# Kernel tuning notes

Hardware: AMD Instinct MI355X
Metric: run time of the kernel (lower is better)

Reference implementation:

```python
import jax, jax.numpy as jnp
import numpy as np

ALPHA = 0.2
NEG_INF = -9e15


def setup_inputs() -> dict:
    key = jax.random.key(0)
    k1, k2, k3, k4 = jax.random.split(key, 4)
    B, N, C_IN, C_OUT, R, H = 8, 1024, 256, 256, 4, 4
    node_feats = jax.random.normal(k1, (B, N, C_IN), dtype=jnp.float32)
    adj_matrix = jax.random.randint(k2, (B, N, N, R), 0, 2, dtype=jnp.int32)
    # xavier_uniform with gain=1.414 for Linear(c_in, c_out) weights
    lim_w = 1.414 * np.sqrt(6.0 / (C_IN + C_OUT))
    W = jax.random.uniform(k3, (R, C_IN, C_OUT), minval=-lim_w, maxval=lim_w, dtype=jnp.float32)
    c_per = C_OUT // H
    lim_a = 1.414 * np.sqrt(6.0 / (H + 2 * c_per))
    a = jax.random.uniform(k4, (R, H, 2 * c_per), minval=-lim_a, maxval=lim_a, dtype=jnp.float32)
    return {"node_feats": node_feats, "adj_matrix": adj_matrix, "W": W, "a": a}


def reference(node_feats, adj_matrix, W, a):
    B, N, _ = node_feats.shape
    R, H = a.shape[0], a.shape[1]
    C = a.shape[2] // 2  # per-head feature dim
    out = jnp.zeros((B, N, H, C), dtype=node_feats.dtype)
    for r in range(R):
        # per-relation projection: [B,N,H,C]
        f = jnp.einsum('bnc,cd->bnd', node_feats, W[r]).reshape(B, N, H, C)
        a_l, a_r = a[r, :, :C], a[r, :, C:]
        # attention logit decomposes: a . [f_i || f_j] = a_l . f_i + a_r . f_j
        li = jnp.einsum('bnhc,hc->bnh', f, a_l)  # source-node term
        lj = jnp.einsum('bnhc,hc->bnh', f, a_r)  # target-node term
        logits = jax.nn.leaky_relu(li[:, :, None, :] + lj[:, None, :, :], ALPHA)  # [B,N,N,H]
        mask = adj_matrix[..., r] != 0  # [B,N,N]
        logits = jnp.where(mask[..., None], logits, NEG_INF)
        probs = jax.nn.softmax(logits, axis=2)
        out = out + jnp.einsum('bijh,bjhc->bihc', probs, f)
    # concat_heads=True
    return out.reshape(B, N, H * C)
```

## Files before the change

### kernel.cpp

```cpp
#include <hip/hip_runtime.h>
#include <math.h>

#define Bsz 8
#define Nn 1024
#define CIN 256
#define COUT 256
#define NR 4
#define NH 4

typedef unsigned short u16;
typedef __attribute__((ext_vector_type(8))) short bf16x8;
typedef __attribute__((ext_vector_type(4))) float f32x4;
typedef __attribute__((ext_vector_type(2))) float f32x2;

#define OFF_LIP (16u << 20)
#define OFF_LJP ((16u << 20) + (512u << 10))
#define OFF_ADJM (17u << 20)
#define OFF_XBF (21u << 20)
#define OFF_WFRAG (25u << 20)
#define OFF_WAL ((25u << 20) + (512u << 10))
#define OFF_WAR ((25u << 20) + (528u << 10))

#define LOG2E 1.4426950408889634f

__device__ __forceinline__ short f2bf(float x) {
  union { float f; unsigned u; } v; v.f = x;
  unsigned r = (v.u + 0x7FFFu + ((v.u >> 16) & 1u)) >> 16;
  return (short)r;
}

__device__ __forceinline__ float fast_exp2(float x) {
#if __has_builtin(__builtin_amdgcn_exp2f)
  return __builtin_amdgcn_exp2f(x);
#else
  return exp2f(x);
#endif
}

__device__ __forceinline__ int sbfe1(unsigned v, int bit) {
#if __has_builtin(__builtin_amdgcn_sbfe)
  return __builtin_amdgcn_sbfe((int)v, bit, 1);
#else
  return ((int)(v << (31 - bit))) >> 31;
#endif
}

__device__ __forceinline__ unsigned perm_hi16(unsigned hi, unsigned lo) {
#if __has_builtin(__builtin_amdgcn_perm)
  return __builtin_amdgcn_perm(hi, lo, 0x07060302u);
#else
  return (lo >> 16) | (hi & 0xFFFF0000u);
#endif
}

__global__ __launch_bounds__(256, 4)
void gatt_packprep(const int4* __restrict__ adj4, const float* __restrict__ W,
                   const float* __restrict__ a, unsigned long long* __restrict__ adjm,
                   u16* __restrict__ Wfrag, float* __restrict__ wa_l,
                   float* __restrict__ wa_r) {
  const int t = threadIdx.x;
  if (blockIdx.x < 32768) {
    const int wid = blockIdx.x * 4 + (t >> 6);
    const int lane = t & 63;
    const int jw = wid & 15;
    const int i = (wid >> 4) & 1023;
    const int b = wid >> 14;
    const int j = jw * 64 + lane;
    const int4 av = adj4[(size_t)(b * Nn + i) * Nn + j];
    const unsigned long long b0 = __ballot(av.x != 0);
    const unsigned long long b1 = __ballot(av.y != 0);
    const unsigned long long b2 = __ballot(av.z != 0);
    const unsigned long long b3 = __ballot(av.w != 0);
    if (lane < 4) {
      unsigned long long v = (lane == 0) ? b0 : (lane == 1) ? b1 : (lane == 2) ? b2 : b3;
      adjm[((size_t)((b * Nn + i) * NR + lane)) * 16 + jw] = v;
    }
  } else if (blockIdx.x < 32768 + 32) {
    const int bid2 = blockIdx.x - 32768;
    const int r = bid2 >> 3, kc = bid2 & 7;
    const int cg = t >> 4, mm = t & 15;
    float wv[32];
#pragma unroll 8
    for (int kk = 0; kk < 32; ++kk)
      wv[kk] = W[(size_t)r * 65536 + (size_t)(kc * 32 + kk) * COUT + t];
    u16* base = Wfrag + (size_t)r * 65536 + (size_t)(cg * 8 + kc) * 512 + mm * 8;
#pragma unroll
    for (int quad = 0; quad < 4; ++quad) {
      u16 pk[8];
#pragma unroll
      for (int e = 0; e < 8; ++e) pk[e] = (u16)f2bf(wv[quad * 8 + e]);
      *(int4*)(base + quad * 128) = *(int4*)pk;
    }
  } else {
    const int cb = blockIdx.x - 32768 - 32;
    const int r = cb >> 2, h = cb & 3;
    float sl = 0.f, sr = 0.f;
    const float* Wp = W + (size_t)r * 65536 + (size_t)t * COUT + h * 64;
    const float* ap = a + r * 512 + h * 128;
#pragma unroll 8
    for (int c = 0; c < 64; ++c) {
      const float wv = Wp[c];
      sl = fmaf(wv, ap[c], sl);
      sr = fmaf(wv, ap[64 + c], sr);
    }
    wa_l[(size_t)cb * CIN + t] = sl;
    wa_r[(size_t)cb * CIN + t] = sr;
  }
}

__global__ __launch_bounds__(256, 4)
void gatt_logitx(const float* __restrict__ X, const float4* __restrict__ wal4,
                 const float4* __restrict__ war4, float* __restrict__ Lip,
                 float* __restrict__ Ljp, u16* __restrict__ Xbf) {
  __shared__ float Xs[16 * 260];
  const int t = threadIdx.x;
  const int row0 = blockIdx.x * 16;
  {
    const int il = t >> 4, kq = t & 15;
    const float4* xp = (const float4*)(X + (size_t)(row0 + il) * CIN + kq * 16);
    float4 v[4];
    u16 pk[16];
#pragma unroll
    for (int u = 0; u < 4; ++u) {
      v[u] = xp[u];
      pk[u * 4 + 0] = (u16)f2bf(v[u].x);
      pk[u * 4 + 1] = (u16)f2bf(v[u].y);
      pk[u * 4 + 2] = (u16)f2bf(v[u].z);
      pk[u * 4 + 3] = (u16)f2bf(v[u].w);
    }
    float4* dst = (float4*)(Xs + il * 260 + kq * 16);
#pragma unroll
    for (int u = 0; u < 4; ++u) dst[u] = v[u];
    u16* xb = Xbf + (size_t)(row0 + il) * CIN + kq * 16;
    *(int4*)xb = *(int4*)pk;
    *(int4*)(xb + 8) = *(int4*)(pk + 8);
  }
  __syncthreads();
  const int rl = t >> 4, combo = t & 15;
  float li = 0.f, lj = 0.f;
#pragma unroll 8
  for (int k4 = 0; k4 < 64; ++k4) {
    const float4 x4 = *(const float4*)(Xs + rl * 260 + k4 * 4);
    const float4 wl = wal4[combo * 64 + k4];
    const float4 wr = war4[combo * 64 + k4];
    li += x4.x * wl.x + x4.y * wl.y + x4.z * wl.z + x4.w * wl.w;
    lj += x4.x * wr.x + x4.y * wr.y + x4.z * wr.z + x4.w * wr.w;
  }
  const int g = row0 + rl, b = g >> 10, n = g & 1023;
  const size_t idx = ((size_t)(combo * Bsz + b)) * Nn + n;
  Lip[idx] = li * LOG2E;
  Ljp[idx] = lj * LOG2E;
}

__global__ __launch_bounds__(256, 4)
void gatt_fgemm(const u16* __restrict__ Xbf, const u16* __restrict__ Wfrag,
                u16* __restrict__ fTf) {
  const int t = threadIdx.x;
  const int r = blockIdx.x & 3, b = (blockIdx.x >> 2) & 7, ntl = blockIdx.x >> 5;
  const int n0 = ntl * 32;
  const int lane = t & 63, w = t >> 6;
  const int m = lane & 15, quad = lane >> 4;

  const u16* wbase = Wfrag + (size_t)r * 65536 + (size_t)(w * 4) * 8 * 512 + lane * 8;
  const u16* xbase = Xbf + (size_t)(b * Nn + n0 + m) * CIN + quad * 8;

  f32x4 acc[4][2];
#pragma unroll
  for (int ct = 0; ct < 4; ++ct)
#pragma unroll
    for (int nt = 0; nt < 2; ++nt) acc[ct][nt] = (f32x4){0.f, 0.f, 0.f, 0.f};

#pragma unroll
  for (int kc = 0; kc < 8; ++kc) {
    bf16x8 af[4], bfr[2];
#pragma unroll
    for (int ct = 0; ct < 4; ++ct)
      af[ct] = *(const bf16x8*)(wbase + (size_t)(ct * 8 + kc) * 512);
#pragma unroll
    for (int nt = 0; nt < 2; ++nt)
      bfr[nt] = *(const bf16x8*)(xbase + (size_t)(nt * 16) * CIN + kc * 32);
#pragma unroll
    for (int ct = 0; ct < 4; ++ct)
#pragma unroll
      for (int nt = 0; nt < 2; ++nt)
        acc[ct][nt] = __builtin_amdgcn_mfma_f32_16x16x32_bf16(af[ct], bfr[nt], acc[ct][nt], 0, 0, 0);
  }

  u16* fragbase = fTf + (size_t)(((r * Bsz + b) * 4 + w) * 128) * 512;
  const int jb = n0 >> 5;
  const int e = m & 7;
#pragma unroll
  for (int ct = 0; ct < 4; ++ct) {
#pragma unroll
    for (int nt = 0; nt < 2; ++nt) {
      const int qt = nt * 2 + (m >> 3);
      u16* dst = fragbase + (size_t)((jb * 4 + ct) * 512) + (qt * 16 + quad * 4) * 8 + e;
#pragma unroll
      for (int p = 0; p < 4; ++p) dst[p * 8] = (u16)f2bf(acc[ct][nt][p]);
    }
  }
}

__global__ __launch_bounds__(512, 4)
void gatt_attn(const unsigned long long* __restrict__ adjm,
               const u16* __restrict__ fTf, const float* __restrict__ Lip,
               const float* __restrict__ Ljp, float* __restrict__ out) {
  __shared__ float lred[8 * 2184];

  const int t = threadIdx.x;
  const int b = blockIdx.x & 7;
  const int hpair = (blockIdx.x >> 3) & 1;
  const int i0 = (blockIdx.x >> 4) * 32;
  const int w = t >> 6, lane = t & 63;
  const int hl = w & 1, r = w >> 1;
  const int h = hpair * 2 + hl;
  const int m = lane & 15, quad = lane >> 4;
  const int qo = quad * 8;

  const float* lipb = Lip + ((size_t)((r * NH + h) * Bsz + b)) * Nn;
  const float li0 = lipb[i0 + m];
  const float li1 = lipb[i0 + 16 + m];
  const float* ljh = Ljp + ((size_t)((r * NH + h) * Bsz + b)) * Nn;
  const unsigned long long* amp0 = adjm + ((size_t)((b * Nn + i0 + m) * NR + r)) * 16;
  const unsigned long long* amp1 = amp0 + (size_t)16 * NR * 16;
  const bf16x8* fp = (const bf16x8*)fTf + (size_t)((r * Bsz + b) * 4 + h) * 8192;

  bf16x8 ones;
#pragma unroll
  for (int e = 0; e < 8; ++e) ones[e] = (short)0x3F80;

  f32x4 acc[2][4], den[2];
#pragma unroll
  for (int iw = 0; iw < 2; ++iw) {
    den[iw] = (f32x4){0.f, 0.f, 0.f, 0.f};
#pragma unroll
    for (int nt = 0; nt < 4; ++nt) acc[iw][nt] = (f32x4){0.f, 0.f, 0.f, 0.f};
  }

  for (int jq = 0; jq < 16; ++jq) {
    const uint2 mw0 = *(const uint2*)(amp0 + jq);
    const uint2 mw1 = *(const uint2*)(amp1 + jq);
#pragma unroll
    for (int half = 0; half < 2; ++half) {
      const int jb = jq * 2 + half;
      const unsigned w0 = half ? mw0.y : mw0.x;
      const unsigned w1 = half ? mw1.y : mw1.x;
      const f32x2* lj2p = (const f32x2*)(ljh + jb * 32 + qo);
      bf16x8 bfr[4];
#pragma unroll
      for (int nt = 0; nt < 4; ++nt) bfr[nt] = fp[(jb * 4 + nt) * 64 + lane];
#pragma unroll
      for (int iw = 0; iw < 2; ++iw) {
        const float liv = iw ? li1 : li0;
        const unsigned mb = (iw ? w1 : w0) >> qo;
        const f32x2 li2 = {liv, liv};
        unsigned afu[4];
#pragma unroll
        for (int pr = 0; pr < 4; ++pr) {
          const f32x2 s2 = li2 + lj2p[pr];
          const f32x2 s02 = s2 * 0.2f;
          const float t0 = fmaxf(s2.x, s02.x);
          const float t1 = fmaxf(s2.y, s02.y);
          const unsigned e0 =
              __float_as_uint(fast_exp2(t0)) & (unsigned)sbfe1(mb, 2 * pr);
          const unsigned e1 =
              __float_as_uint(fast_exp2(t1)) & (unsigned)sbfe1(mb, 2 * pr + 1);
          afu[pr] = perm_hi16(e1, e0);
        }
        union { unsigned u[4]; bf16x8 v; } af;
        af.u[0] = afu[0]; af.u[1] = afu[1]; af.u[2] = afu[2]; af.u[3] = afu[3];
        den[iw] = __builtin_amdgcn_mfma_f32_16x16x32_bf16(af.v, ones, den[iw], 0, 0, 0);
#pragma unroll
        for (int nt = 0; nt < 4; ++nt)
          acc[iw][nt] = __builtin_amdgcn_mfma_f32_16x16x32_bf16(af.v, bfr[nt], acc[iw][nt], 0, 0, 0);
      }
    }
  }

  float* ltile = lred + (hl * 4 + r) * 2184;
#pragma unroll
  for (int iw = 0; iw < 2; ++iw) {
#pragma unroll
    for (int p = 0; p < 4; ++p) {
      const float inv = __builtin_amdgcn_rcpf(den[iw][p]);
      float* lp = ltile + (iw * 16 + quad * 4 + p) * 68 + m;
#pragma unroll
      for (int nt = 0; nt < 4; ++nt) lp[nt * 16] = acc[iw][nt][p] * inv;
    }
  }
  __syncthreads();

  {
    const int ci = t >> 4;
    const int cc = (t & 15) * 8;
    const int chl = cc >> 6;
    const int cin = cc & 63;
    const float* basep = lred + chl * 4 * 2184 + ci * 68 + cin;
    f32x4 s0 = (f32x4){0.f, 0.f, 0.f, 0.f};
    f32x4 s1 = (f32x4){0.f, 0.f, 0.f, 0.f};
#pragma unroll
    for (int rr = 0; rr < 4; ++rr) {
      const f32x4 a0 = *(const f32x4*)(basep + rr * 2184);
      const f32x4 a1 = *(const f32x4*)(basep + rr * 2184 + 4);
      s0 += a0;
      s1 += a1;
    }
    float* op = out + ((size_t)(b * Nn) + i0 + ci) * COUT + hpair * 128 + cc;
    *(f32x4*)op = s0;
    *(f32x4*)(op + 4) = s1;
  }
}

extern "C" void kernel_launch(void* const* d_in, const int* in_sizes, int n_in,
                              void* d_out, int out_size, void* d_ws, size_t ws_size,
                              hipStream_t stream) {
  const float* X = (const float*)d_in[0];
  const int4* adj4 = (const int4*)d_in[1];
  const float* W = (const float*)d_in[2];
  const float* a = (const float*)d_in[3];
  float* out = (float*)d_out;

  char* ws = (char*)d_ws;
  u16* fTf = (u16*)ws;
  float* Lip = (float*)(ws + OFF_LIP);
  float* Ljp = (float*)(ws + OFF_LJP);
  unsigned long long* adjm = (unsigned long long*)(ws + OFF_ADJM);
  u16* Xbf = (u16*)(ws + OFF_XBF);
  u16* Wfrag = (u16*)(ws + OFF_WFRAG);
  float* wa_l = (float*)(ws + OFF_WAL);
  float* wa_r = (float*)(ws + OFF_WAR);

  gatt_packprep<<<dim3(32816), dim3(256), 0, stream>>>(adj4, W, a, adjm, Wfrag,
                                                       wa_l, wa_r);
  gatt_logitx<<<dim3(512), dim3(256), 0, stream>>>(X, (const float4*)wa_l,
                                                   (const float4*)wa_r, Lip, Ljp, Xbf);
  gatt_fgemm<<<dim3(1024), dim3(256), 0, stream>>>(Xbf, Wfrag, fTf);
  gatt_attn<<<dim3(512), dim3(512), 0, stream>>>(adjm, fTf, Lip, Ljp, out);
}
```

Before: 296.1 us.

## Split attention j-range across wave pairs, one head per block, LDS atomic reduce

The attention kernel now gives each block a single head and doubles the grid. The two waves per relation each handle half of the neighbour (j) range. Partial numerators and denominators are merged with LDS atomicAdd into a zeroed shared tile, and the normalisation is moved to after the reduction. LDS use per block is smaller and the launch bound allows 6 blocks, which aims to raise occupancy and expose more parallelism, at the cost of LDS atomics, a zeroing pass and an extra barrier.

```diff
diff --git a/kernel.cpp b/kernel.cpp
--- a/kernel.cpp
+++ b/kernel.cpp
@@ -201,21 +201,25 @@
   }
 }
 
-__global__ __launch_bounds__(512, 4)
+#define TSTRIDE 2184
+#define DEN_OFF (4 * TSTRIDE)
+__global__ __launch_bounds__(512, 6)
 void gatt_attn(const unsigned long long* __restrict__ adjm,
                const u16* __restrict__ fTf, const float* __restrict__ Lip,
                const float* __restrict__ Ljp, float* __restrict__ out) {
-  __shared__ float lred[8 * 2184];
+  __shared__ float lred[4 * TSTRIDE + 128];
 
   const int t = threadIdx.x;
   const int b = blockIdx.x & 7;
-  const int hpair = (blockIdx.x >> 3) & 1;
-  const int i0 = (blockIdx.x >> 4) * 32;
+  const int h = (blockIdx.x >> 3) & 3;
+  const int i0 = (blockIdx.x >> 5) * 32;
   const int w = t >> 6, lane = t & 63;
-  const int hl = w & 1, r = w >> 1;
-  const int h = hpair * 2 + hl;
+  const int r = w >> 1, jh = w & 1;
   const int m = lane & 15, quad = lane >> 4;
   const int qo = quad * 8;
+
+  for (int s = t; s < 4 * TSTRIDE + 128; s += 512) lred[s] = 0.f;
+  __syncthreads();
 
   const float* lipb = Lip + ((size_t)((r * NH + h) * Bsz + b)) * Nn;
   const float li0 = lipb[i0 + m];
@@ -237,7 +241,9 @@
     for (int nt = 0; nt < 4; ++nt) acc[iw][nt] = (f32x4){0.f, 0.f, 0.f, 0.f};
   }
 
-  for (int jq = 0; jq < 16; ++jq) {
+  const int jq0 = jh * 8;
+#pragma unroll 2
+  for (int jq = jq0; jq < jq0 + 8; ++jq) {
     const uint2 mw0 = *(const uint2*)(amp0 + jq);
     const uint2 mw1 = *(const uint2*)(amp1 + jq);
 #pragma unroll
@@ -277,37 +283,38 @@
     }
   }
 
-  float* ltile = lred + (hl * 4 + r) * 2184;
-#pragma unroll
-  for (int iw = 0; iw < 2; ++iw) {
-#pragma unroll
-    for (int p = 0; p < 4; ++p) {
-      const float inv = __builtin_amdgcn_rcpf(den[iw][p]);
-      float* lp = ltile + (iw * 16 + quad * 4 + p) * 68 + m;
-#pragma unroll
-      for (int nt = 0; nt < 4; ++nt) lp[nt * 16] = acc[iw][nt][p] * inv;
+  {
+    float* ltile = lred + r * TSTRIDE;
+#pragma unroll
+    for (int iw = 0; iw < 2; ++iw) {
+#pragma unroll
+      for (int p = 0; p < 4; ++p) {
+        float* lp = ltile + (iw * 16 + quad * 4 + p) * 68 + m;
+#pragma unroll
+        for (int nt = 0; nt < 4; ++nt) atomicAdd(lp + nt * 16, acc[iw][nt][p]);
+      }
+    }
+    if (m == 0) {
+#pragma unroll
+      for (int iw = 0; iw < 2; ++iw)
+#pragma unroll
+        for (int p = 0; p < 4; ++p)
+          atomicAdd(lred + DEN_OFF + r * 32 + iw * 16 + quad * 4 + p, den[iw][p]);
     }
   }
   __syncthreads();
 
   {
     const int ci = t >> 4;
-    const int cc = (t & 15) * 8;
-    const int chl = cc >> 6;
-    const int cin = cc & 63;
-    const float* basep = lred + chl * 4 * 2184 + ci * 68 + cin;
-    f32x4 s0 = (f32x4){0.f, 0.f, 0.f, 0.f};
-    f32x4 s1 = (f32x4){0.f, 0.f, 0.f, 0.f};
+    const int cc = (t & 15) * 4;
+    f32x4 s = (f32x4){0.f, 0.f, 0.f, 0.f};
 #pragma unroll
     for (int rr = 0; rr < 4; ++rr) {
-      const f32x4 a0 = *(const f32x4*)(basep + rr * 2184);
-      const f32x4 a1 = *(const f32x4*)(basep + rr * 2184 + 4);
-      s0 += a0;
-      s1 += a1;
-    }
-    float* op = out + ((size_t)(b * Nn) + i0 + ci) * COUT + hpair * 128 + cc;
-    *(f32x4*)op = s0;
-    *(f32x4*)(op + 4) = s1;
+      const f32x4 v = *(const f32x4*)(lred + rr * TSTRIDE + ci * 68 + cc);
+      const float inv = __builtin_amdgcn_rcpf(lred[DEN_OFF + rr * 32 + ci]);
+      s += v * inv;
+    }
+    *(f32x4*)(out + ((size_t)(b * Nn) + i0 + ci) * COUT + h * 64 + cc) = s;
   }
 }
 
@@ -335,5 +342,5 @@
   gatt_logitx<<<dim3(512), dim3(256), 0, stream>>>(X, (const float4*)wa_l,
                                                    (const float4*)wa_r, Lip, Ljp, Xbf);
   gatt_fgemm<<<dim3(1024), dim3(256), 0, stream>>>(Xbf, Wfrag, fTf);
-  gatt_attn<<<dim3(512), dim3(512), 0, stream>>>(adjm, fTf, Lip, Ljp, out);
-}
+  gatt_attn<<<dim3(1024), dim3(512), 0, stream>>>(adjm, fTf, Lip, Ljp, out);
+}
```

New measurement: 446.2 us. 50.7% more time.
